# Kernel optimization log

Measured on AMD Instinct MI355X. Metric: run time of the kernel, lower is better.

The kernel has to match this reference:

```python
import jax, jax.numpy as jnp
import numpy as np
from jax import lax

B, S, H, E, K = 2, 1024, 2048, 16, 4
CAP = int(B * S * 1.5 * K / E)  # capacity = 768
ALPHA = 0.7

def _mlp2(x, w1, b1, w2, b2):
    return jnp.maximum(x @ w1 + b1, 0.0) @ w2 + b2

def setup_inputs() -> dict:
    key = jax.random.key(0)
    ks = iter(jax.random.split(key, 32))
    def w(shape, scale=0.02):
        return (jax.random.normal(next(ks), shape, dtype=jnp.float32) * scale)
    inp = {
        'hidden_states': jax.random.normal(next(ks), (B, S, H), dtype=jnp.float32),
        'mod_image': jax.random.normal(next(ks), (B, S, H), dtype=jnp.float32),
        'mod_genomic': jax.random.normal(next(ks), (B, S, H), dtype=jnp.float32),
        'g_w1': w((H, H)), 'g_b1': jnp.zeros((H,), jnp.float32),
        'g_w2': w((H, E)), 'g_b2': jnp.zeros((E,), jnp.float32),
        'm_w1': w((H, H)), 'm_b1': jnp.zeros((H,), jnp.float32),
        'm_w2': w((H, H)), 'm_b2': jnp.zeros((H,), jnp.float32),
    }
    for p in ('si', 'sg', 'sc', 'sb'):
        inp[p + '_w1'] = w((H, H // 2)); inp[p + '_b1'] = jnp.zeros((H // 2,), jnp.float32)
        inp[p + '_w2'] = w((H // 2, E)); inp[p + '_b2'] = jnp.zeros((E,), jnp.float32)
    return inp

def reference(hidden_states, mod_image, mod_genomic,
              g_w1, g_b1, g_w2, g_b2,
              si_w1, si_b1, si_w2, si_b2,
              sg_w1, sg_b1, sg_w2, sg_b2,
              sc_w1, sc_b1, sc_w2, sc_b2,
              sb_w1, sb_b1, sb_w2, sb_b2,
              m_w1, m_b1, m_w2, m_b2):
    # generalized router probs over experts
    g_probs = jax.nn.softmax(_mlp2(hidden_states, g_w1, g_b1, g_w2, g_b2), axis=-1)
    # missing-modality representation (clinical + biospecimen are missing)
    miss = _mlp2(hidden_states, m_w1, m_b1, m_w2, m_b2)
    # specialized routers: image, genomic (available) + clinical, biospecimen (use miss)
    s_probs = (jax.nn.softmax(_mlp2(mod_image, si_w1, si_b1, si_w2, si_b2), axis=-1)
               + jax.nn.softmax(_mlp2(mod_genomic, sg_w1, sg_b1, sg_w2, sg_b2), axis=-1)
               + jax.nn.softmax(_mlp2(miss, sc_w1, sc_b1, sc_w2, sc_b2), axis=-1)
               + jax.nn.softmax(_mlp2(miss, sb_w1, sb_b1, sb_w2, sb_b2), axis=-1))
    s_probs = s_probs / 2.0  # divided by len(available_modalities) == 2, as in source
    router_probs = ALPHA * g_probs + (1.0 - ALPHA) * s_probs  # [B,S,E]
    top_k_probs, top_k_idx = lax.top_k(router_probs, K)  # [B,S,K]
    top_k_probs = top_k_probs / top_k_probs.sum(axis=-1, keepdims=True)
    onehot = jax.nn.one_hot(top_k_idx, E, dtype=router_probs.dtype)  # [B,S,K,E]
    dmask = onehot.sum(axis=-2)                               # [B,S,E] (0/1: experts distinct)
    cmask = (onehot * top_k_probs[..., None]).sum(axis=-2)    # [B,S,E]
    dispatch = jnp.zeros((B, S, E, CAP), router_probs.dtype).at[..., 0].set(dmask)
    combine = jnp.zeros((B, S, E, CAP), router_probs.dtype).at[..., 0].set(cmask)
    mean_probs = router_probs.mean(axis=(0, 1))  # [E]
    aux_loss = jnp.sum(mean_probs * jnp.log(mean_probs * E + 1e-9))
    return dispatch, combine, router_probs, aux_loss
```

## Files before the change

### kernel.cpp

```cpp
#include <hip/hip_runtime.h>
#include <math.h>
#include <stdint.h>

#define NTOK 2048
#define HDIM 2048
#define HHALF 1024
#define EDIM 16
#define CAPV 768
#define TOPK 4
#define GK 2048

typedef __bf16 bf16x8 __attribute__((ext_vector_type(8)));
typedef __bf16 bf16x4 __attribute__((ext_vector_type(4)));
typedef float f32x4 __attribute__((ext_vector_type(4)));


struct GJobA {
  const __bf16 *Ah, *Al, *Wh, *Wl;
  const float* bias;
  float* Cf; __bf16 *Ch, *Cl;
  int relu, N, blk0;
};
struct GJobsA { GJobA j[6]; };

#define BKA 32
#define NTA 64

#define BARR __builtin_amdgcn_s_barrier()
#define SCHED0 __builtin_amdgcn_sched_barrier(0)
#define PRIO1 __builtin_amdgcn_s_setprio(1)
#define PRIO0 __builtin_amdgcn_s_setprio(0)

__global__ __launch_bounds__(512, 2) void gemm_phased(GJobsA P) {
  __shared__ __align__(16) __bf16 lds[2][4][256 * BKA];

  const int tid = threadIdx.x;
  const int wid = tid >> 6, lane = tid & 63;
  const int lane15 = lane & 15, c0 = lane >> 4;

  const int bid = blockIdx.x;
  int ji = 0;
#pragma unroll
  for (int k = 1; k < 6; ++k)
    if (bid >= P.j[k].blk0) ji = k;
  const GJobA J = P.j[ji];
  const int local = bid - J.blk0;
  const int nbx = J.N >> 8;
  const int bx = local & (nbx - 1);
  const int by = local / nbx;
  const int m0 = by * 256, n0 = bx * 256;

  const int wr = wid >> 2, wc = wid & 3;

  int srow[2], soff[2];
#pragma unroll
  for (int h = 0; h < 2; ++h) {
    int s = tid + h * 512;
    int row = s >> 2;
    srow[h] = row;
    soff[h] = ((s & 3) ^ ((row >> 1) & 3)) * 8;
  }

  int offB[4], offA[2][4];
#pragma unroll
  for (int ni = 0; ni < 4; ++ni) {
    int rb = wc * 64 + ni * 16 + lane15;
    offB[ni] = rb * 64 + ((c0 ^ ((rb >> 1) & 3)) << 4);
  }
#pragma unroll
  for (int mh = 0; mh < 2; ++mh)
#pragma unroll
    for (int i = 0; i < 4; ++i) {
      int ra = wr * 128 + mh * 64 + i * 16 + lane15;
      offA[mh][i] = ra * 64 + ((c0 ^ ((ra >> 1) & 3)) << 4);
    }

#define STAGE2(gptr, grow0, k1, larr)                                          \
  { _Pragma("unroll") for (int h = 0; h < 2; ++h) {                            \
      const __bf16* _src =                                                     \
          (gptr) + (size_t)((grow0) + srow[h]) * GK + (k1) + soff[h];          \
      __builtin_amdgcn_global_load_lds(                                        \
          (const __attribute__((address_space(1))) uint32_t*)_src,             \
          (__attribute__((address_space(3))) uint32_t*)((larr) +               \
              (wid * 64 + h * 512) * 8), 16, 0, 0); } }

#define DSR_A(dst, base, h)                                                    \
  { _Pragma("unroll") for (int i = 0; i < 4; ++i)                              \
      dst[i] = *(const bf16x8*)((base) + offA[h][i]); }
#define DSR_B(dst, base)                                                       \
  { _Pragma("unroll") for (int i = 0; i < 4; ++i)                              \
      dst[i] = *(const bf16x8*)((base) + offB[i]); }
#define MFMA16(af, bf, mh)                                                     \
  { _Pragma("unroll") for (int mi = 0; mi < 4; ++mi)                           \
    _Pragma("unroll") for (int ni = 0; ni < 4; ++ni)                           \
      acc[(mh) * 4 + mi][ni] = __builtin_amdgcn_mfma_f32_16x16x32_bf16(        \
          af[mi], bf[ni], acc[(mh) * 4 + mi][ni], 0, 0, 0); }

  f32x4 acc[8][4];
#pragma unroll
  for (int i = 0; i < 8; ++i)
#pragma unroll
    for (int j = 0; j < 4; ++j) acc[i][j] = (f32x4){0.f, 0.f, 0.f, 0.f};

  STAGE2(J.Ah, m0, 0, lds[0][0]);
  STAGE2(J.Wh, n0, 0, lds[0][2]);
  STAGE2(J.Wl, n0, 0, lds[0][3]);
  STAGE2(J.Al, m0, 0, lds[0][1]);
  asm volatile("s_waitcnt vmcnt(2)" ::: "memory");
  BARR;
  SCHED0;

  bf16x8 ah[4], al[4], bh[4], bl[4];

  for (int t = 0; t < NTA; ++t) {
    const int cur = t & 1, nxt = cur ^ 1;
    const bool hasNext = (t + 1 < NTA);
    const int k1 = (t + 1) * BKA;
    const char* cAh = (const char*)lds[cur][0];
    const char* cAl = (const char*)lds[cur][1];
    const char* cBh = (const char*)lds[cur][2];
    const char* cBl = (const char*)lds[cur][3];

    if (hasNext) {
      STAGE2(J.Ah, m0, k1, lds[nxt][0]);
      STAGE2(J.Wh, n0, k1, lds[nxt][2]);
    }
    DSR_A(ah, cAh, 0);
    DSR_B(bh, cBh);
    DSR_B(bl, cBl);
    PRIO1; MFMA16(ah, bh, 0); PRIO0;
    if (hasNext) { asm volatile("s_waitcnt vmcnt(4)" ::: "memory"); }
    else         { asm volatile("s_waitcnt vmcnt(0)" ::: "memory"); }
    SCHED0;
    BARR;
    SCHED0;
    if (hasNext) {
      STAGE2(J.Wl, n0, k1, lds[nxt][3]);
      STAGE2(J.Al, m0, k1, lds[nxt][1]);
    }
    DSR_A(al, cAl, 0);
    PRIO1; MFMA16(ah, bl, 0); PRIO0;
    DSR_A(ah, cAh, 1);
    PRIO1; MFMA16(al, bh, 0); PRIO0;
    DSR_A(al, cAl, 1);
    PRIO1; MFMA16(ah, bh, 1); PRIO0;
    PRIO1; MFMA16(ah, bl, 1); MFMA16(al, bh, 1); PRIO0;
    if (hasNext) {
      asm volatile("s_waitcnt vmcnt(2)" ::: "memory");
      SCHED0;
      BARR;
      SCHED0;
    }
  }

#pragma unroll
  for (int mh = 0; mh < 2; ++mh)
#pragma unroll
    for (int mi = 0; mi < 4; ++mi)
#pragma unroll
      for (int ni = 0; ni < 4; ++ni) {
        int col = n0 + wc * 64 + ni * 16 + lane15;
        float bv = J.bias[col];
        f32x4 v = acc[mh * 4 + mi][ni];
#pragma unroll
        for (int j = 0; j < 4; ++j) {
          int row = m0 + wr * 128 + mh * 64 + mi * 16 + c0 * 4 + j;
          float x = v[j] + bv;
          if (J.relu) x = fmaxf(x, 0.0f);
          size_t o = (size_t)row * J.N + col;
          if (J.Cf) J.Cf[o] = x;
          if (J.Ch) {
            __bf16 hh = (__bf16)x;
            J.Ch[o] = hh;
            J.Cl[o] = (__bf16)(x - (float)hh);
          }
        }
      }
#undef STAGE2
#undef DSR_A
#undef DSR_B
#undef MFMA16
}

#define BKT 64

struct GJob {
  const __bf16* Ah; const __bf16* Al;
  const __bf16* Wh; const __bf16* Wl;
  const float* bias;
  float* Cf;
  int N; int blk0; int kLen;
};
struct LJob3 { const float* Y; const float* W2; const float* b2; float* L; int K; };
struct StageBArgs { GJob gj[4]; LJob3 lj[3]; };

__global__ __launch_bounds__(256) void stageB(StageBArgs P) {
  __shared__ __align__(16) __bf16 lds[4 * 128 * BKT];
  const int bid = blockIdx.x;
  const int tid = threadIdx.x;

  if (bid >= 512) {
    const int lid = bid - 512;
    const LJob3 J = P.lj[lid >> 8];
    const int blk = lid & 255;
    const int wid = tid >> 6, lane = tid & 63;
    const int e = lane & 15;
    const int kq = lane >> 4;
    const int tok0 = blk * 8 + wid * 2;
    const float* y0 = J.Y + (size_t)tok0 * J.K;
    const float* y1 = y0 + J.K;
    const int KQ = J.K >> 2;
    const int kbase = kq * KQ;
    float a0 = 0.f, a1 = 0.f;
#pragma unroll 8
    for (int k = 0; k < KQ; ++k) {
      int kk = kbase + k;
      float w = J.W2[(size_t)kk * EDIM + e];
      a0 = fmaf(y0[kk], w, a0);
      a1 = fmaf(y1[kk], w, a1);
    }
    a0 += __shfl_xor(a0, 16); a0 += __shfl_xor(a0, 32);
    a1 += __shfl_xor(a1, 16); a1 += __shfl_xor(a1, 32);
    if (lane < 16) {
      float b = J.b2[e];
      J.L[(size_t)tok0 * EDIM + e] = a0 + b;
      J.L[(size_t)(tok0 + 1) * EDIM + e] = a1 + b;
    }
    return;
  }

  __bf16* ldsAh = lds;
  __bf16* ldsAl = lds + 8192;
  __bf16* ldsBh = lds + 16384;
  __bf16* ldsBl = lds + 24576;
  const char* cAh = (const char*)ldsAh;
  const char* cAl = (const char*)ldsAl;
  const char* cBh = (const char*)ldsBh;
  const char* cBl = (const char*)ldsBl;

  int ji = 0;
#pragma unroll
  for (int k = 1; k < 4; ++k)
    if (bid >= P.gj[k].blk0) ji = k;
  const GJob J = P.gj[ji];
  const int local = bid - J.blk0;
  const int nbx = J.N >> 7;
  const int bx = local & (nbx - 1);
  const int by = local / nbx;
  const int m0 = by * 128;
  const int n0 = bx * 128;

  const int wid = tid >> 6;
  const int lane = tid & 63;
  const int lane15 = lane & 15;
  const int c0 = lane >> 4;
  const int wr = wid >> 1;
  const int wc = wid & 1;

  int offA[4][2], offB[4][2];
#pragma unroll
  for (int i = 0; i < 4; ++i) {
    int ra = wr * 64 + i * 16 + lane15;
    int rb = wc * 64 + i * 16 + lane15;
#pragma unroll
    for (int ks = 0; ks < 2; ++ks) {
      offA[i][ks] = ra * 128 + (((ks * 4 + c0) ^ (ra & 7)) << 4);
      offB[i][ks] = rb * 128 + (((ks * 4 + c0) ^ (rb & 7)) << 4);
    }
  }

  f32x4 acc[4][4];
#pragma unroll
  for (int i = 0; i < 4; ++i)
#pragma unroll
    for (int j = 0; j < 4; ++j) acc[i][j] = (f32x4){0.f, 0.f, 0.f, 0.f};

  const int r_in = lane >> 3;
  const int swz_elems = ((lane & 7) ^ r_in) << 3;
#define STG(gptr, grow0, k0, lbase)                                            \
  { _Pragma("unroll") for (int i = 0; i < 4; ++i) {                            \
      int row0 = wid * 32 + i * 8;                                             \
      const __bf16* src =                                                      \
          (gptr) + (size_t)((grow0) + row0 + r_in) * GK + (k0) + swz_elems;    \
      __builtin_amdgcn_global_load_lds(                                        \
          (const __attribute__((address_space(1))) uint32_t*)src,              \
          (__attribute__((address_space(3))) uint32_t*)((lbase) + row0 * BKT), \
          16, 0, 0); } }

  for (int k0 = 0; k0 < J.kLen; k0 += BKT) {
    STG(J.Ah, m0, k0, ldsAh);
    STG(J.Al, m0, k0, ldsAl);
    STG(J.Wh, n0, k0, ldsBh);
    STG(J.Wl, n0, k0, ldsBl);
    __syncthreads();
#pragma unroll
    for (int ks = 0; ks < 2; ++ks) {
      bf16x8 ah[4], al[4], bh[4], bl[4];
#pragma unroll
      for (int i = 0; i < 4; ++i) {
        ah[i] = *(const bf16x8*)(cAh + offA[i][ks]);
        al[i] = *(const bf16x8*)(cAl + offA[i][ks]);
        bh[i] = *(const bf16x8*)(cBh + offB[i][ks]);
        bl[i] = *(const bf16x8*)(cBl + offB[i][ks]);
      }
#pragma unroll
      for (int mi = 0; mi < 4; ++mi)
#pragma unroll
        for (int ni = 0; ni < 4; ++ni) {
          acc[mi][ni] = __builtin_amdgcn_mfma_f32_16x16x32_bf16(
              ah[mi], bh[ni], acc[mi][ni], 0, 0, 0);
          acc[mi][ni] = __builtin_amdgcn_mfma_f32_16x16x32_bf16(
              ah[mi], bl[ni], acc[mi][ni], 0, 0, 0);
          acc[mi][ni] = __builtin_amdgcn_mfma_f32_16x16x32_bf16(
              al[mi], bh[ni], acc[mi][ni], 0, 0, 0);
        }
    }
    __syncthreads();
  }
#undef STG

#pragma unroll
  for (int mi = 0; mi < 4; ++mi) {
#pragma unroll
    for (int ni = 0; ni < 4; ++ni) {
      int col = n0 + wc * 64 + ni * 16 + lane15;
      float bv = J.bias[col];
      f32x4 v = acc[mi][ni];
#pragma unroll
      for (int j = 0; j < 4; ++j) {
        int row = m0 + wr * 64 + mi * 16 + c0 * 4 + j;
        float x = v[j] + bv;
        J.Cf[(size_t)row * J.N + col] = x;
      }
    }
  }
}

struct SJob { const float* in; __bf16* h; __bf16* l; };
struct TJob { const float* W; __bf16* Th; __bf16* Tl; int Nd; };
struct PrepArgs {
  float* dout; int out_size; int zb;
  SJob s[4];
  TJob t[6];
  const float* pb2;
  const float* pW1a; const float* pb1a; float* pva;
  const float* pW1b; const float* pb1b; float* pvb;
};

__global__ __launch_bounds__(256) void prep(PrepArgs P) {
  __shared__ float tbuf[32][33];
  const int bid = blockIdx.x;
  const int tid = threadIdx.x;
  if (bid < P.zb) {
    const int n4 = P.out_size >> 2;
    float4 z = {0.f, 0.f, 0.f, 0.f};
#pragma unroll
    for (int it = 0; it < 4; ++it) {
      int i = bid * 1024 + it * 256 + tid;
      if (i < n4) ((float4*)P.dout)[i] = z;
    }
    if (bid == 0 && tid < 4) {
      int i = (n4 << 2) + tid;
      if (i < P.out_size) P.dout[i] = 0.0f;
    }
    return;
  }
  const int rb = bid - P.zb;
  if (rb < 16384) {
    SJob J = P.s[rb >> 12];
    int i = (rb & 4095) * 256 + tid;
    float4 v = ((const float4*)J.in)[i];
    bf16x4 hv, lv;
    hv.x = (__bf16)v.x; lv.x = (__bf16)(v.x - (float)hv.x);
    hv.y = (__bf16)v.y; lv.y = (__bf16)(v.y - (float)hv.y);
    hv.z = (__bf16)v.z; lv.z = (__bf16)(v.z - (float)hv.z);
    hv.w = (__bf16)v.w; lv.w = (__bf16)(v.w - (float)hv.w);
    ((bf16x4*)J.h)[i] = hv;
    ((bf16x4*)J.l)[i] = lv;
  } else if (rb < 32768) {
    int local = rb - 16384;
    int ji, ln;
    if (local < 4096)      { ji = 0; ln = local; }
    else if (local < 8192) { ji = 1; ln = local - 4096; }
    else { ji = 2 + ((local - 8192) >> 11); ln = (local - 8192) & 2047; }
    TJob J = P.t[ji];
    int full = (J.Nd == HDIM);
    int n0 = (full ? (ln & 63) : (ln & 31)) * 32;
    int k0 = (full ? (ln >> 6) : (ln >> 5)) * 32;
    int tx = tid & 31, ty = tid >> 5;
#pragma unroll
    for (int i = 0; i < 4; ++i) {
      int kk = ty + i * 8;
      tbuf[kk][tx] = J.W[(size_t)(k0 + kk) * J.Nd + n0 + tx];
    }
    __syncthreads();
#pragma unroll
    for (int i = 0; i < 4; ++i) {
      int nn = ty + i * 8;
      float v = tbuf[tx][nn];
      __bf16 hh = (__bf16)v;
      size_t o = (size_t)(n0 + nn) * GK + k0 + tx;
      J.Th[o] = hh;
      J.Tl[o] = (__bf16)(v - (float)hh);
    }
  } else {
    int local = rb - 32768;
    int side = local >> 5; int r = local & 31;
    const float* W1 = side ? P.pW1b : P.pW1a;
    const float* b1 = side ? P.pb1b : P.pb1a;
    float* v = side ? P.pvb : P.pva;
    int n = (r & 3) * 256 + tid;
    int k0 = (r >> 2) * 256;
    float acc = (k0 == 0) ? b1[n] : 0.0f;
#pragma unroll 8
    for (int k = 0; k < 256; ++k)
      acc = fmaf(P.pb2[k0 + k], W1[(size_t)(k0 + k) * HHALF + n], acc);
    atomicAdd(&v[n], acc);
  }
}

struct LJob { const float* Y; const float* Y2; const float* W2;
              const float* b2; float* L; };
struct LJobs { LJob j[2]; };
__global__ __launch_bounds__(256) void logits_kernel(LJobs P) {
  const LJob J = P.j[blockIdx.x >> 8];
  const int blk = blockIdx.x & 255;
  const int tid = threadIdx.x;
  const int wid = tid >> 6, lane = tid & 63;
  const int e = lane & 15;
  const int kq = lane >> 4;
  const int tok0 = blk * 8 + wid * 2;
  const float* y0 = J.Y + (size_t)tok0 * HHALF;
  const float* y1 = y0 + HHALF;
  const float* z0 = J.Y2 + (size_t)tok0 * HHALF;
  const float* z1 = z0 + HHALF;
  const int KQ = HHALF >> 2;
  const int kbase = kq * KQ;
  float a0 = 0.f, a1 = 0.f;
#pragma unroll 8
  for (int k = 0; k < KQ; ++k) {
    int kk = kbase + k;
    float w = J.W2[(size_t)kk * EDIM + e];
    float v0 = fmaxf(y0[kk] + z0[kk], 0.0f);
    float v1 = fmaxf(y1[kk] + z1[kk], 0.0f);
    a0 = fmaf(v0, w, a0);
    a1 = fmaf(v1, w, a1);
  }
  a0 += __shfl_xor(a0, 16); a0 += __shfl_xor(a0, 32);
  a1 += __shfl_xor(a1, 16); a1 += __shfl_xor(a1, 32);
  if (lane < 16) {
    float b = J.b2[e];
    J.L[(size_t)tok0 * EDIM + e] = a0 + b;
    J.L[(size_t)(tok0 + 1) * EDIM + e] = a1 + b;
  }
}

__device__ __forceinline__ void softmax16(const float* __restrict__ L, float* __restrict__ p) {
  float v[16];
  *(float4*)&v[0]  = *(const float4*)&L[0];
  *(float4*)&v[4]  = *(const float4*)&L[4];
  *(float4*)&v[8]  = *(const float4*)&L[8];
  *(float4*)&v[12] = *(const float4*)&L[12];
  float m = v[0];
#pragma unroll
  for (int e = 1; e < 16; ++e) m = fmaxf(m, v[e]);
  float s = 0.0f;
#pragma unroll
  for (int e = 0; e < 16; ++e) { v[e] = expf(v[e] - m); s += v[e]; }
  float inv = 1.0f / s;
#pragma unroll
  for (int e = 0; e < 16; ++e) p[e] = v[e] * inv;
}

__global__ __launch_bounds__(256) void finalize_kernel(
    const float* __restrict__ Lg, const float* __restrict__ Lsi,
    const float* __restrict__ Lsg, const float* __restrict__ Lsc,
    const float* __restrict__ Lsb,
    float* __restrict__ dispatch, float* __restrict__ combine,
    float* __restrict__ router_probs, float* __restrict__ mean_acc) {
  __shared__ float sm[EDIM];
  int tid = threadIdx.x;
  if (tid < EDIM) sm[tid] = 0.0f;
  __syncthreads();

  int tok = blockIdx.x * 256 + tid;
  float pg[16], ps[16], tmp[16], r[16];
  softmax16(Lg + (size_t)tok * EDIM, pg);
  softmax16(Lsi + (size_t)tok * EDIM, ps);
  softmax16(Lsg + (size_t)tok * EDIM, tmp);
#pragma unroll
  for (int e = 0; e < 16; ++e) ps[e] += tmp[e];
  softmax16(Lsc + (size_t)tok * EDIM, tmp);
#pragma unroll
  for (int e = 0; e < 16; ++e) ps[e] += tmp[e];
  softmax16(Lsb + (size_t)tok * EDIM, tmp);
#pragma unroll
  for (int e = 0; e < 16; ++e) ps[e] += tmp[e];

#pragma unroll
  for (int e = 0; e < 16; ++e) {
    float s = ps[e] * 0.5f;
    r[e] = 0.7f * pg[e] + 0.3f * s;
  }

#pragma unroll
  for (int e = 0; e < 16; e += 4) {
    float4 o = {r[e], r[e + 1], r[e + 2], r[e + 3]};
    *(float4*)&router_probs[(size_t)tok * EDIM + e] = o;
  }

#pragma unroll
  for (int e = 0; e < 16; ++e) atomicAdd(&sm[e], r[e]);

  bool used[16];
#pragma unroll
  for (int e = 0; e < 16; ++e) used[e] = false;
  int idx[TOPK];
  float tp[TOPK];
  float tsum = 0.0f;
#pragma unroll
  for (int j = 0; j < TOPK; ++j) {
    float best = -1.0f;
    int bi = 0;
#pragma unroll
    for (int e = 0; e < 16; ++e) {
      bool take = (!used[e]) && (r[e] > best);
      best = take ? r[e] : best;
      bi = take ? e : bi;
    }
    used[bi] = true;
    idx[j] = bi;
    tp[j] = best;
    tsum += best;
  }
  float invt = 1.0f / tsum;
#pragma unroll
  for (int j = 0; j < TOPK; ++j) {
    size_t off = ((size_t)tok * EDIM + idx[j]) * CAPV;
    dispatch[off] = 1.0f;
    combine[off] = tp[j] * invt;
  }

  __syncthreads();
  if (tid < EDIM) atomicAdd(&mean_acc[tid], sm[tid]);
}

__global__ void aux_kernel(const float* __restrict__ mean_acc, float* __restrict__ out_aux) {
  if (threadIdx.x == 0 && blockIdx.x == 0) {
    float s = 0.0f;
    for (int e = 0; e < EDIM; ++e) {
      float m = mean_acc[e] * (1.0f / (float)NTOK);
      s += m * logf(m * (float)EDIM + 1e-9f);
    }
    *out_aux = s;
  }
}

#define MBYTE (1ull << 20)

extern "C" void kernel_launch(void* const* d_in, const int* in_sizes, int n_in,
                              void* d_out, int out_size, void* d_ws, size_t ws_size,
                              hipStream_t stream) {
  const float* X    = (const float*)d_in[0];
  const float* IMG  = (const float*)d_in[1];
  const float* GEN  = (const float*)d_in[2];
  const float* g_w1 = (const float*)d_in[3];
  const float* g_b1 = (const float*)d_in[4];
  const float* g_w2 = (const float*)d_in[5];
  const float* g_b2 = (const float*)d_in[6];
  const float* m_w1 = (const float*)d_in[7];
  const float* m_b1 = (const float*)d_in[8];
  const float* m_w2 = (const float*)d_in[9];
  const float* m_b2 = (const float*)d_in[10];
  const float* si_w1 = (const float*)d_in[11];
  const float* si_b1 = (const float*)d_in[12];
  const float* si_w2 = (const float*)d_in[13];
  const float* si_b2 = (const float*)d_in[14];
  const float* sg_w1 = (const float*)d_in[15];
  const float* sg_b1 = (const float*)d_in[16];
  const float* sg_w2 = (const float*)d_in[17];
  const float* sg_b2 = (const float*)d_in[18];
  const float* sc_w1 = (const float*)d_in[19];
  const float* sc_b1 = (const float*)d_in[20];
  const float* sc_w2 = (const float*)d_in[21];
  const float* sc_b2 = (const float*)d_in[22];
  const float* sb_w1 = (const float*)d_in[23];
  const float* sb_b1 = (const float*)d_in[24];
  const float* sb_w2 = (const float*)d_in[25];
  const float* sb_b2 = (const float*)d_in[26];

  char* wsb = (char*)d_ws;
  __bf16* Xh    = (__bf16*)(wsb + 0 * MBYTE);
  __bf16* Xl    = (__bf16*)(wsb + 8 * MBYTE);
  __bf16* IMGh  = (__bf16*)(wsb + 16 * MBYTE);
  __bf16* IMGl  = (__bf16*)(wsb + 24 * MBYTE);
  __bf16* GENh  = (__bf16*)(wsb + 32 * MBYTE);
  __bf16* GENl  = (__bf16*)(wsb + 40 * MBYTE);
  __bf16* M2h   = (__bf16*)(wsb + 48 * MBYTE);
  __bf16* M2l   = (__bf16*)(wsb + 56 * MBYTE);
  __bf16* Wm1h  = (__bf16*)(wsb + 64 * MBYTE);
  __bf16* Wm1l  = (__bf16*)(wsb + 72 * MBYTE);
  __bf16* Wg1h  = (__bf16*)(wsb + 80 * MBYTE);
  __bf16* Wg1l  = (__bf16*)(wsb + 88 * MBYTE);
  __bf16* Wsch  = (__bf16*)(wsb + 96 * MBYTE);
  __bf16* Wscl  = (__bf16*)(wsb + 100 * MBYTE);
  __bf16* Wsbh  = (__bf16*)(wsb + 104 * MBYTE);
  __bf16* Wsbl  = (__bf16*)(wsb + 108 * MBYTE);
  __bf16* Wsih  = (__bf16*)(wsb + 112 * MBYTE);
  __bf16* Wsil  = (__bf16*)(wsb + 116 * MBYTE);
  __bf16* Wsgh  = (__bf16*)(wsb + 120 * MBYTE);
  __bf16* Wsgl  = (__bf16*)(wsb + 124 * MBYTE);
  __bf16* H1h   = (__bf16*)(wsb + 128 * MBYTE);
  __bf16* H1l   = (__bf16*)(wsb + 136 * MBYTE);
  __bf16* WPsch = (__bf16*)(wsb + 144 * MBYTE);
  __bf16* WPscl = (__bf16*)(wsb + 148 * MBYTE);
  __bf16* WPsbh = (__bf16*)(wsb + 152 * MBYTE);
  __bf16* WPsbl = (__bf16*)(wsb + 156 * MBYTE);
  float*  YG    = (float*)(wsb + 160 * MBYTE);
  float*  YSI   = (float*)(wsb + 176 * MBYTE);
  float*  YSG   = (float*)(wsb + 184 * MBYTE);
  float*  YSCp0 = (float*)(wsb + 192 * MBYTE);
  float*  YSCp1 = (float*)(wsb + 200 * MBYTE);
  float*  YSBp0 = (float*)(wsb + 208 * MBYTE);
  float*  YSBp1 = (float*)(wsb + 216 * MBYTE);
  float* L0 = (float*)(wsb + 224 * MBYTE);
  float* L1 = L0 + NTOK * EDIM;
  float* L2 = L1 + NTOK * EDIM;
  float* L3 = L2 + NTOK * EDIM;
  float* L4 = L3 + NTOK * EDIM;
  float* meanp = L4 + NTOK * EDIM;
  float* zbias = meanp + EDIM;
  float* vsc = zbias + GK;
  float* vsb = vsc + HHALF;

  float* dispatch = (float*)d_out;
  float* combine = dispatch + (size_t)NTOK * EDIM * CAPV;
  float* rp = combine + (size_t)NTOK * EDIM * CAPV;
  float* aux = rp + (size_t)NTOK * EDIM;

  hipMemsetAsync(meanp, 0, (EDIM + GK + 2 * HHALF) * sizeof(float), stream);

  dim3 blk(256);
  const int zb = (out_size + 4095) / 4096;

  {
    PrepArgs p;
    p.dout = (float*)d_out; p.out_size = out_size; p.zb = zb;
    p.s[0] = {X, Xh, Xl};
    p.s[1] = {IMG, IMGh, IMGl};
    p.s[2] = {GEN, GENh, GENl};
    p.s[3] = {m_w2, M2h, M2l};
    p.t[0] = {m_w1, Wm1h, Wm1l, HDIM};
    p.t[1] = {g_w1, Wg1h, Wg1l, HDIM};
    p.t[2] = {sc_w1, Wsch, Wscl, HHALF};
    p.t[3] = {sb_w1, Wsbh, Wsbl, HHALF};
    p.t[4] = {si_w1, Wsih, Wsil, HHALF};
    p.t[5] = {sg_w1, Wsgh, Wsgl, HHALF};
    p.pb2 = m_b2;
    p.pW1a = sc_w1; p.pb1a = sc_b1; p.pva = vsc;
    p.pW1b = sb_w1; p.pb1b = sb_b1; p.pvb = vsb;
    prep<<<zb + 32832, blk, 0, stream>>>(p);
  }

  {
    GJobsA g;
    g.j[0] = {Xh, Xl, Wm1h, Wm1l, m_b1, nullptr, H1h, H1l, 1, HDIM, 0};
    g.j[1] = {Xh, Xl, Wg1h, Wg1l, g_b1, YG, nullptr, nullptr, 1, HDIM, 64};
    g.j[2] = {IMGh, IMGl, Wsih, Wsil, si_b1, YSI, nullptr, nullptr, 1, HHALF, 128};
    g.j[3] = {GENh, GENl, Wsgh, Wsgl, sg_b1, YSG, nullptr, nullptr, 1, HHALF, 160};
    g.j[4] = {Wsch, Wscl, M2h, M2l, zbias, nullptr, WPsch, WPscl, 0, HDIM, 192};
    g.j[5] = {Wsbh, Wsbl, M2h, M2l, zbias, nullptr, WPsbh, WPsbl, 0, HDIM, 224};
    gemm_phased<<<256, dim3(512), 0, stream>>>(g);
  }

  {
    StageBArgs s;
    s.gj[0] = {H1h, H1l, WPsch, WPscl, vsc, YSCp0, HHALF, 0, 1024};
    s.gj[1] = {H1h + 1024, H1l + 1024, WPsch + 1024, WPscl + 1024, zbias, YSCp1,
               HHALF, 128, 1024};
    s.gj[2] = {H1h, H1l, WPsbh, WPsbl, vsb, YSBp0, HHALF, 256, 1024};
    s.gj[3] = {H1h + 1024, H1l + 1024, WPsbh + 1024, WPsbl + 1024, zbias, YSBp1,
               HHALF, 384, 1024};
    s.lj[0] = {YG, g_w2, g_b2, L0, HDIM};
    s.lj[1] = {YSI, si_w2, si_b2, L1, HHALF};
    s.lj[2] = {YSG, sg_w2, sg_b2, L2, HHALF};
    stageB<<<512 + 768, blk, 0, stream>>>(s);
  }

  {
    LJobs l;
    l.j[0] = {YSCp0, YSCp1, sc_w2, sc_b2, L3};
    l.j[1] = {YSBp0, YSBp1, sb_w2, sb_b2, L4};
    logits_kernel<<<2 * 256, blk, 0, stream>>>(l);
  }

  finalize_kernel<<<NTOK / 256, blk, 0, stream>>>(L0, L1, L2, L3, L4,
                                                  dispatch, combine, rp, meanp);
  aux_kernel<<<1, 64, 0, stream>>>(meanp, aux);
}
```

Before: 405.0 us.

## Swizzle GEMM block order, coarsen split prep, zero output via memset

The two GEMM kernels now remap block indices with an XCD-aware swizzle, so neighbouring tiles that share operands land on the same chiplet and reuse its L2. The prep kernel no longer zeroes the large dispatch/combine output inside its own blocks; that is now a hipMemsetAsync, which may use a faster fill path. The bf16 hi/lo split now handles four float4s per thread, which cuts the block count. Together these aim to reduce the large memory-fill cost and improve cache locality, at the cost of an extra API call and a changed block mapping.

```diff
diff --git a/kernel.cpp b/kernel.cpp
--- a/kernel.cpp
+++ b/kernel.cpp
@@ -38,7 +38,7 @@
   const int wid = tid >> 6, lane = tid & 63;
   const int lane15 = lane & 15, c0 = lane >> 4;
 
-  const int bid = blockIdx.x;
+  const int bid = (blockIdx.x & 7) * 32 + (blockIdx.x >> 3);
   int ji = 0;
 #pragma unroll
   for (int k = 1; k < 6; ++k)
@@ -196,11 +196,10 @@
 
 __global__ __launch_bounds__(256) void stageB(StageBArgs P) {
   __shared__ __align__(16) __bf16 lds[4 * 128 * BKT];
-  const int bid = blockIdx.x;
   const int tid = threadIdx.x;
 
-  if (bid >= 512) {
-    const int lid = bid - 512;
+  if (blockIdx.x >= 512) {
+    const int lid = blockIdx.x - 512;
     const LJob3 J = P.lj[lid >> 8];
     const int blk = lid & 255;
     const int wid = tid >> 6, lane = tid & 63;
@@ -229,6 +228,7 @@
     return;
   }
 
+  const int bid = ((blockIdx.x & 7) * 64 + (blockIdx.x >> 3));
   __bf16* ldsAh = lds;
   __bf16* ldsAl = lds + 8192;
   __bf16* ldsBh = lds + 16384;
@@ -339,7 +339,6 @@
 struct SJob { const float* in; __bf16* h; __bf16* l; };
 struct TJob { const float* W; __bf16* Th; __bf16* Tl; int Nd; };
 struct PrepArgs {
-  float* dout; int out_size; int zb;
   SJob s[4];
   TJob t[6];
   const float* pb2;
@@ -351,34 +350,23 @@
   __shared__ float tbuf[32][33];
   const int bid = blockIdx.x;
   const int tid = threadIdx.x;
-  if (bid < P.zb) {
-    const int n4 = P.out_size >> 2;
-    float4 z = {0.f, 0.f, 0.f, 0.f};
+  if (bid < 4096) {
+    SJob J = P.s[bid >> 10];
+    int base = (bid & 1023) * 1024 + tid;
 #pragma unroll
     for (int it = 0; it < 4; ++it) {
-      int i = bid * 1024 + it * 256 + tid;
-      if (i < n4) ((float4*)P.dout)[i] = z;
-    }
-    if (bid == 0 && tid < 4) {
-      int i = (n4 << 2) + tid;
-      if (i < P.out_size) P.dout[i] = 0.0f;
-    }
-    return;
-  }
-  const int rb = bid - P.zb;
-  if (rb < 16384) {
-    SJob J = P.s[rb >> 12];
-    int i = (rb & 4095) * 256 + tid;
-    float4 v = ((const float4*)J.in)[i];
-    bf16x4 hv, lv;
-    hv.x = (__bf16)v.x; lv.x = (__bf16)(v.x - (float)hv.x);
-    hv.y = (__bf16)v.y; lv.y = (__bf16)(v.y - (float)hv.y);
-    hv.z = (__bf16)v.z; lv.z = (__bf16)(v.z - (float)hv.z);
-    hv.w = (__bf16)v.w; lv.w = (__bf16)(v.w - (float)hv.w);
-    ((bf16x4*)J.h)[i] = hv;
-    ((bf16x4*)J.l)[i] = lv;
-  } else if (rb < 32768) {
-    int local = rb - 16384;
+      int i = base + it * 256;
+      float4 v = ((const float4*)J.in)[i];
+      bf16x4 hv, lv;
+      hv.x = (__bf16)v.x; lv.x = (__bf16)(v.x - (float)hv.x);
+      hv.y = (__bf16)v.y; lv.y = (__bf16)(v.y - (float)hv.y);
+      hv.z = (__bf16)v.z; lv.z = (__bf16)(v.z - (float)hv.z);
+      hv.w = (__bf16)v.w; lv.w = (__bf16)(v.w - (float)hv.w);
+      ((bf16x4*)J.h)[i] = hv;
+      ((bf16x4*)J.l)[i] = lv;
+    }
+  } else if (bid < 20480) {
+    int local = bid - 4096;
     int ji, ln;
     if (local < 4096)      { ji = 0; ln = local; }
     else if (local < 8192) { ji = 1; ln = local - 4096; }
@@ -404,7 +392,7 @@
       J.Tl[o] = (__bf16)(v - (float)hh);
     }
   } else {
-    int local = rb - 32768;
+    int local = bid - 20480;
     int side = local >> 5; int r = local & 31;
     const float* W1 = side ? P.pW1b : P.pW1a;
     const float* b1 = side ? P.pb1b : P.pb1a;
@@ -638,14 +626,13 @@
   float* rp = combine + (size_t)NTOK * EDIM * CAPV;
   float* aux = rp + (size_t)NTOK * EDIM;
 
+  hipMemsetAsync(d_out, 0, (size_t)out_size * sizeof(float), stream);
   hipMemsetAsync(meanp, 0, (EDIM + GK + 2 * HHALF) * sizeof(float), stream);
 
   dim3 blk(256);
-  const int zb = (out_size + 4095) / 4096;
 
   {
     PrepArgs p;
-    p.dout = (float*)d_out; p.out_size = out_size; p.zb = zb;
     p.s[0] = {X, Xh, Xl};
     p.s[1] = {IMG, IMGh, IMGl};
     p.s[2] = {GEN, GENh, GENl};
@@ -659,7 +646,7 @@
     p.pb2 = m_b2;
     p.pW1a = sc_w1; p.pb1a = sc_b1; p.pva = vsc;
     p.pW1b = sb_w1; p.pb1b = sb_b1; p.pvb = vsb;
-    prep<<<zb + 32832, blk, 0, stream>>>(p);
+    prep<<<20544, blk, 0, stream>>>(p);
   }
 
   {
```

After: 407.1 us. About the same (+0.5%).
